# Kernel tuning notes

Measured on AMD Instinct MI355X. Metric: run time of the kernel, lower is better.

The kernel has to match this reference:

```python
import jax, jax.numpy as jnp
import numpy as np

D_MODEL = 2048
HQ = 32
HK = 8
DK = D_MODEL // HQ  # 64
G = HQ // HK        # 4
VOCAB = 32000
B, S = 1, 2048


def setup_inputs() -> dict:
    key = jax.random.key(0)
    ks = jax.random.split(key, 7)
    scale = 1.0 / np.sqrt(D_MODEL)
    X = jax.random.randint(ks[0], (B, S), 0, VOCAB, dtype=jnp.int64)
    emb = jax.random.normal(ks[1], (VOCAB, D_MODEL), dtype=jnp.float32)
    Wk = jax.random.normal(ks[2], (HK * DK, D_MODEL), dtype=jnp.float32) * scale
    Wv = jax.random.normal(ks[3], (HK * DK, D_MODEL), dtype=jnp.float32) * scale
    Wq = jax.random.normal(ks[4], (D_MODEL, D_MODEL), dtype=jnp.float32) * scale
    Wo_w = jax.random.normal(ks[5], (D_MODEL, D_MODEL), dtype=jnp.float32) * scale
    Wo_b = jax.random.normal(ks[6], (D_MODEL,), dtype=jnp.float32) * scale
    return {"X": X, "emb": emb, "Wk": Wk, "Wv": Wv, "Wq": Wq, "Wo_w": Wo_w, "Wo_b": Wo_b}


def reference(X, emb, Wk, Wv, Wq, Wo_w, Wo_b):
    e = emb[X]  # [B,S,D]
    b, s, _ = e.shape
    # torch Linear: y = x @ W.T (weights stored [out,in])
    k = (e @ Wk.T).reshape(b, s, HK, DK)            # [B,S,Hk,dk]
    v = (e @ Wv.T).reshape(b, s, HK, DK)            # [B,S,Hk,dk]
    q = (e @ Wq.T).reshape(b, s, HK, G, DK)         # q head index = i*G + g
    # scores: [B,Hk,G,S,S] — same math as expanding KV to Hq heads, no copy
    scores = jnp.einsum('bsigd,btid->bigst', q, k) / jnp.sqrt(jnp.asarray(DK, e.dtype))
    w = jax.nn.softmax(scores, axis=-1)
    ctx = jnp.einsum('bigst,btid->bsigd', w, v).reshape(b, s, D_MODEL)
    return ctx @ Wo_w.T + Wo_b
```

## Files before the change

kernel.cpp:

```cpp
#include <hip/hip_runtime.h>


typedef __bf16 bf16x8 __attribute__((ext_vector_type(8)));
typedef float f32x4 __attribute__((ext_vector_type(4)));
typedef float f32x16 __attribute__((ext_vector_type(16)));
typedef unsigned short ushort8_t __attribute__((ext_vector_type(8)));
typedef unsigned int uint4_t __attribute__((ext_vector_type(4)));

#define DEVI static __device__ __forceinline__

DEVI unsigned short f2bf(float f) {
    union { float f; unsigned int u; } c; c.f = f;
    unsigned int u = c.u;
    unsigned int r = (u + 0x7FFFu + ((u >> 16) & 1u)) >> 16;
    return (unsigned short)r;
}

DEVI f32x4 mfma16(bf16x8 a, bf16x8 b, f32x4 c) {
    return __builtin_amdgcn_mfma_f32_16x16x32_bf16(a, b, c, 0, 0, 0);
}
DEVI f32x16 mfma32(bf16x8 a, bf16x8 b, f32x16 c) {
    return __builtin_amdgcn_mfma_f32_32x32x16_bf16(a, b, c, 0, 0, 0);
}
DEVI unsigned cvtpk(float a, float b) {
    unsigned r;
    asm("v_cvt_pk_bf16_f32 %0, %1, %2" : "=v"(r) : "v"(a), "v"(b));
    return r;
}
DEVI void plswap(unsigned& a, unsigned& b) {
    asm("v_permlane32_swap_b32 %0, %1" : "+v"(a), "+v"(b));
}
DEVI void gload16(const unsigned short* g, unsigned short* l) {
    __builtin_amdgcn_global_load_lds(
        (const __attribute__((address_space(1))) void*)g,
        (__attribute__((address_space(3))) void*)l, 16, 0, 0);
}
#define WAIT_VM(n) asm volatile("s_waitcnt vmcnt(" #n ")" ::: "memory")
#define WAIT_LGKM0() asm volatile("s_waitcnt lgkmcnt(0)" ::: "memory")
#define BAR() __builtin_amdgcn_s_barrier()

DEVI void cvt8(const float* src, unsigned short* dst) {
    float4 f0 = *(const float4*)(src);
    float4 f1 = *(const float4*)(src + 4);
    ushort8_t v;
    v[0] = f2bf(f0.x); v[1] = f2bf(f0.y); v[2] = f2bf(f0.z); v[3] = f2bf(f0.w);
    v[4] = f2bf(f1.x); v[5] = f2bf(f1.y); v[6] = f2bf(f1.z); v[7] = f2bf(f1.w);
    *(ushort8_t*)(dst) = v;
}

__global__ __launch_bounds__(256)
void prep_k(const int* __restrict__ X, const float* __restrict__ emb,
            unsigned short* __restrict__ e,
            const float* __restrict__ Wk, unsigned short* __restrict__ Wkb,
            const float* __restrict__ Wv, unsigned short* __restrict__ Wvb,
            const float* __restrict__ Wq, unsigned short* __restrict__ Wqb,
            const float* __restrict__ Wo, unsigned short* __restrict__ Wob) {
    int b = blockIdx.x;
    if (b < 2048) {
        long long row = X[b];
        cvt8(emb + row * 2048 + threadIdx.x * 8, e + (size_t)b * 2048 + threadIdx.x * 8);
        return;
    }
    b -= 2048;
    const float* s; unsigned short* d; int off;
    if (b < 512) { s = Wk; d = Wkb; off = b; }
    else if (b < 1024) { s = Wv; d = Wvb; off = b - 512; }
    else if (b < 3072) { s = Wq; d = Wqb; off = b - 1024; }
    else { s = Wo; d = Wob; off = b - 3072; }
    size_t idx = ((size_t)off * 256 + threadIdx.x) * 8;
    cvt8(s + idx, d + idx);
}

template<int OM0, int OM1, int OM2>
__global__ __launch_bounds__(256)
void gemm_swz_k(const unsigned short* __restrict__ A,
                const unsigned short* __restrict__ W0, const unsigned short* __restrict__ W1,
                const unsigned short* __restrict__ W2,
                void* __restrict__ C0, void* __restrict__ C1, void* __restrict__ C2,
                int t1, int t2, int ldc0, int ldc1, int ldc2,
                const float* __restrict__ bias) {
    __shared__ unsigned short As[2 * 128 * 64];
    __shared__ unsigned short Bs[2 * 128 * 64];
    const int cpx = gridDim.x >> 3;
    int id = blockIdx.x;
    int swz = (id & 7) * cpx + (id >> 3);
    const int bx = swz & 15;
    const int by = swz >> 4;
    const unsigned short* Wp; void* Cp; int ldc, om, nb;
    if (by < t1)      { Wp = W0; Cp = C0; ldc = ldc0; om = OM0; nb = by; }
    else if (by < t2) { Wp = W1; Cp = C1; ldc = ldc1; om = OM1; nb = by - t1; }
    else              { Wp = W2; Cp = C2; ldc = ldc2; om = OM2; nb = by - t2; }
    const int m0 = bx * 128, n0 = nb * 128;
    const int tid = threadIdx.x, lane = tid & 63, w = tid >> 6;
    const int wm = (w >> 1) * 64, wn = (w & 1) * 64;
    const int lr = lane & 15, lg = lane >> 4;
    const int srow = tid >> 3, sj = tid & 7;

    f32x4 acc[4][4];
    #pragma unroll
    for (int i = 0; i < 4; i++)
        #pragma unroll
        for (int j = 0; j < 4; j++) acc[i][j] = {};

    #define G_STAGE(buf, k0)                                                          \
        _Pragma("unroll")                                                             \
        for (int i = 0; i < 4; i++) {                                                 \
            int row = srow + i * 32;                                                  \
            int jj = sj ^ (row & 7);                                                  \
            unsigned short* ad = As + (buf) * 8192 + (w * 64 + i * 256) * 8;          \
            unsigned short* bd = Bs + (buf) * 8192 + (w * 64 + i * 256) * 8;          \
            gload16(A  + (size_t)(m0 + row) * 2048 + (k0) + jj * 8, ad);              \
            gload16(Wp + (size_t)(n0 + row) * 2048 + (k0) + jj * 8, bd);              \
        }

    G_STAGE(0, 0);
    for (int s = 0; s < 32; ++s) {
        const int cur = s & 1;
        if (s < 31) {
            G_STAGE(cur ^ 1, (s + 1) * 64);
            WAIT_VM(8);
        } else {
            WAIT_VM(0);
        }
        BAR();
        const unsigned short* Asb = As + cur * 8192;
        const unsigned short* Bsb = Bs + cur * 8192;
        #pragma unroll
        for (int kk = 0; kk < 2; kk++) {
            bf16x8 af[4], bfr[4];
            #pragma unroll
            for (int mi = 0; mi < 4; mi++) {
                int r = wm + mi * 16 + lr;
                int g = (kk * 4 + lg) ^ (r & 7);
                af[mi] = *(const bf16x8*)(&Asb[r * 64 + g * 8]);
            }
            #pragma unroll
            for (int ni = 0; ni < 4; ni++) {
                int r = wn + ni * 16 + lr;
                int g = (kk * 4 + lg) ^ (r & 7);
                bfr[ni] = *(const bf16x8*)(&Bsb[r * 64 + g * 8]);
            }
            __builtin_amdgcn_s_setprio(1);
            #pragma unroll
            for (int mi = 0; mi < 4; mi++)
                #pragma unroll
                for (int ni = 0; ni < 4; ni++)
                    acc[mi][ni] = mfma16(af[mi], bfr[ni], acc[mi][ni]);
            __builtin_amdgcn_s_setprio(0);
        }
        WAIT_LGKM0();
        BAR();
    }
    #undef G_STAGE

    #pragma unroll
    for (int mi = 0; mi < 4; mi++)
        #pragma unroll
        for (int ni = 0; ni < 4; ni++) {
            int col = n0 + wn + ni * 16 + lr;
            #pragma unroll
            for (int jj = 0; jj < 4; jj++) {
                int rowg = m0 + wm + mi * 16 + lg * 4 + jj;
                float vv = acc[mi][ni][jj];
                if (om == 0) {
                    ((unsigned short*)Cp)[(size_t)rowg * ldc + col] = f2bf(vv);
                } else if (om == 1) {
                    ((float*)Cp)[(size_t)rowg * ldc + col] = vv + bias[col];
                } else {
                    ((unsigned short*)Cp)[(size_t)col * ldc + rowg] = f2bf(vv);
                }
            }
        }
}

__global__ __launch_bounds__(256)
void attn2_k(const unsigned short* __restrict__ Qb, const unsigned short* __restrict__ Kb,
             const unsigned short* __restrict__ VbT, unsigned short* __restrict__ Ctx) {
    __shared__ unsigned short Ks[2 * 64 * 64];
    __shared__ unsigned short Vts[2 * 64 * 64];
    int id = blockIdx.x;
    int swz = (id & 7) * 64 + (id >> 3);
    const int hq = swz >> 4;
    const int qt = swz & 15;
    const int ikv = hq >> 2;
    const int tid = threadIdx.x, lane = tid & 63, w = tid >> 6;
    const int l31 = lane & 31, hi = lane >> 5;
    const int qrow = qt * 128 + w * 32 + l31;
    const float CS = 0.125f * 1.44269504088896f;
    const int srow = tid >> 3, sj = tid & 7;

    bf16x8 qf[4];
    #pragma unroll
    for (int ks = 0; ks < 4; ks++)
        qf[ks] = *(const bf16x8*)(Qb + (size_t)qrow * 2048 + hq * 64 + ks * 16 + hi * 8);

    f32x16 oacc0 = {}, oacc1 = {};
    float m = -1e30f, l = 0.0f;

    #define A_STAGE(buf, t0)                                                          \
        _Pragma("unroll")                                                             \
        for (int i = 0; i < 2; i++) {                                                 \
            int row = srow + i * 32;                                                  \
            int jj = sj ^ (row & 7);                                                  \
            unsigned short* kd = Ks + (buf) * 4096 + (w * 64 + i * 256) * 8;          \
            unsigned short* vd = Vts + (buf) * 4096 + (w * 64 + i * 256) * 8;         \
            gload16(Kb + (size_t)((t0) + row) * 512 + ikv * 64 + jj * 8, kd);         \
            gload16(VbT + (size_t)(ikv * 64 + row) * 2048 + (t0) + jj * 8, vd);       \
        }

    A_STAGE(0, 0);
    for (int t = 0; t < 32; ++t) {
        const int cur = t & 1;
        if (t < 31) {
            A_STAGE(cur ^ 1, (t + 1) * 64);
            WAIT_VM(4);
        } else {
            WAIT_VM(0);
        }
        BAR();
        const unsigned short* Ksb = Ks + cur * 4096;
        const unsigned short* Vsb = Vts + cur * 4096;

        f32x16 s0 = {}, s1 = {};
        __builtin_amdgcn_s_setprio(1);
        #pragma unroll
        for (int ks = 0; ks < 4; ks++) {
            int gr = (2 * ks + hi) ^ (l31 & 7);
            bf16x8 kf0 = *(const bf16x8*)(&Ksb[l31 * 64 + gr * 8]);
            bf16x8 kf1 = *(const bf16x8*)(&Ksb[(32 + l31) * 64 + gr * 8]);
            s0 = mfma32(kf0, qf[ks], s0);
            s1 = mfma32(kf1, qf[ks], s1);
        }
        __builtin_amdgcn_s_setprio(0);

        float mx[8];
        #pragma unroll
        for (int r = 0; r < 8; r++)
            mx[r] = fmaxf(fmaxf(s0[2 * r], s0[2 * r + 1]),
                          fmaxf(s1[2 * r], s1[2 * r + 1]));
        #pragma unroll
        for (int st = 4; st > 0; st >>= 1)
            #pragma unroll
            for (int r = 0; r < st; r++) mx[r] = fmaxf(mx[r], mx[r + st]);
        float pmax = fmaxf(mx[0], __shfl_xor(mx[0], 32, 64));
        pmax *= CS;

        if (!__all(pmax <= m + 8.0f)) {
            float mnew = fmaxf(m, pmax);
            float sc = exp2f(m - mnew);
            m = mnew;
            l *= sc;
            #pragma unroll
            for (int r = 0; r < 16; r++) {
                const int qp = (r & 3) + 8 * (r >> 2);
                float scv = __shfl(sc, qp + 4 * hi, 64);
                oacc0[r] *= scv;
                oacc1[r] *= scv;
            }
        }

        float rs0 = 0.f, rs1 = 0.f, rs2 = 0.f, rs3 = 0.f;
        #pragma unroll
        for (int r = 0; r < 16; r += 4) {
            float p0 = exp2f(__builtin_fmaf(s0[r],     CS, -m)); s0[r]     = p0; rs0 += p0;
            float p1 = exp2f(__builtin_fmaf(s0[r + 1], CS, -m)); s0[r + 1] = p1; rs1 += p1;
            float p2 = exp2f(__builtin_fmaf(s0[r + 2], CS, -m)); s0[r + 2] = p2; rs2 += p2;
            float p3 = exp2f(__builtin_fmaf(s0[r + 3], CS, -m)); s0[r + 3] = p3; rs3 += p3;
        }
        #pragma unroll
        for (int r = 0; r < 16; r += 4) {
            float p0 = exp2f(__builtin_fmaf(s1[r],     CS, -m)); s1[r]     = p0; rs0 += p0;
            float p1 = exp2f(__builtin_fmaf(s1[r + 1], CS, -m)); s1[r + 1] = p1; rs1 += p1;
            float p2 = exp2f(__builtin_fmaf(s1[r + 2], CS, -m)); s1[r + 2] = p2; rs2 += p2;
            float p3 = exp2f(__builtin_fmaf(s1[r + 3], CS, -m)); s1[r + 3] = p3; rs3 += p3;
        }
        float rs = (rs0 + rs1) + (rs2 + rs3);
        rs += __shfl_xor(rs, 32, 64);
        l += rs;

        uint4_t pw[4];
        #pragma unroll
        for (int c = 0; c < 2; c++) {
            unsigned a   = cvtpk(s0[8 * c + 0], s0[8 * c + 1]);
            unsigned bb  = cvtpk(s0[8 * c + 2], s0[8 * c + 3]);
            unsigned cc2 = cvtpk(s0[8 * c + 4], s0[8 * c + 5]);
            unsigned dd  = cvtpk(s0[8 * c + 6], s0[8 * c + 7]);
            plswap(a, cc2); plswap(bb, dd);
            pw[c][0] = a; pw[c][1] = bb; pw[c][2] = cc2; pw[c][3] = dd;
        }
        #pragma unroll
        for (int c = 0; c < 2; c++) {
            unsigned a   = cvtpk(s1[8 * c + 0], s1[8 * c + 1]);
            unsigned bb  = cvtpk(s1[8 * c + 2], s1[8 * c + 3]);
            unsigned cc2 = cvtpk(s1[8 * c + 4], s1[8 * c + 5]);
            unsigned dd  = cvtpk(s1[8 * c + 6], s1[8 * c + 7]);
            plswap(a, cc2); plswap(bb, dd);
            pw[2 + c][0] = a; pw[2 + c][1] = bb; pw[2 + c][2] = cc2; pw[2 + c][3] = dd;
        }

        __builtin_amdgcn_s_setprio(1);
        #pragma unroll
        for (int ks = 0; ks < 4; ks++) {
            bf16x8 pa = __builtin_bit_cast(bf16x8, pw[ks]);
            int gr = (2 * ks + hi) ^ (l31 & 7);
            bf16x8 vf0 = *(const bf16x8*)(&Vsb[l31 * 64 + gr * 8]);
            bf16x8 vf1 = *(const bf16x8*)(&Vsb[(32 + l31) * 64 + gr * 8]);
            oacc0 = mfma32(pa, vf0, oacc0);
            oacc1 = mfma32(pa, vf1, oacc1);
        }
        __builtin_amdgcn_s_setprio(0);
        WAIT_LGKM0();
        BAR();
    }
    #undef A_STAGE

    float linv = 1.0f / l;
    #pragma unroll
    for (int r = 0; r < 16; r++) {
        const int qp = (r & 3) + 8 * (r >> 2);
        float lv = __shfl(linv, qp + 4 * hi, 64);
        int row = qt * 128 + w * 32 + qp + 4 * hi;
        Ctx[(size_t)row * 2048 + hq * 64 + l31]      = f2bf(oacc0[r] * lv);
        Ctx[(size_t)row * 2048 + hq * 64 + 32 + l31] = f2bf(oacc1[r] * lv);
    }
}

extern "C" void kernel_launch(void* const* d_in, const int* in_sizes, int n_in,
                              void* d_out, int out_size, void* d_ws, size_t ws_size,
                              hipStream_t stream) {
    (void)in_sizes; (void)n_in; (void)out_size; (void)ws_size;
    const int*   X   = (const int*)d_in[0];
    const float* emb = (const float*)d_in[1];
    const float* Wk  = (const float*)d_in[2];
    const float* Wv  = (const float*)d_in[3];
    const float* Wq  = (const float*)d_in[4];
    const float* Wo  = (const float*)d_in[5];
    const float* Wb  = (const float*)d_in[6];

    unsigned short* e   = (unsigned short*)d_ws;
    unsigned short* Kb  = e   + (size_t)2048 * 2048;
    unsigned short* VbT = Kb  + (size_t)2048 * 512;
    unsigned short* Qb  = VbT + (size_t)512 * 2048;
    unsigned short* Ctx = Qb  + (size_t)2048 * 2048;
    unsigned short* Wkb = Ctx + (size_t)2048 * 2048;
    unsigned short* Wvb = Wkb + (size_t)512 * 2048;
    unsigned short* Wqb = Wvb + (size_t)512 * 2048;
    unsigned short* Wob = Wqb + (size_t)2048 * 2048;

    prep_k<<<dim3(2048 + 5120), dim3(256), 0, stream>>>(X, emb, e, Wk, Wkb, Wv, Wvb,
                                                        Wq, Wqb, Wo, Wob);
    gemm_swz_k<0, 0, 2><<<dim3(384), dim3(256), 0, stream>>>(
        e, Wqb, Wkb, Wvb, (void*)Qb, (void*)Kb, (void*)VbT,
        16, 20, 2048, 512, 2048, nullptr);
    attn2_k<<<dim3(512), dim3(256), 0, stream>>>(Qb, Kb, VbT, Ctx);
    gemm_swz_k<1, 1, 1><<<dim3(256), dim3(256), 0, stream>>>(
        Ctx, Wob, Wob, Wob, d_out, d_out, d_out,
        16, 32, 2048, 2048, 2048, Wb);
}
```

Before: 166.2 us.

## Fold softmax scale into Q projection and compute row sums via MFMA

```diff
diff --git a/kernel.cpp b/kernel.cpp
--- a/kernel.cpp
+++ b/kernel.cpp
@@ -8,6 +8,8 @@
 typedef unsigned int uint4_t __attribute__((ext_vector_type(4)));
 
 #define DEVI static __device__ __forceinline__
+
+#define QSCALE 0.180336880111112f
 
 DEVI unsigned short f2bf(float f) {
     union { float f; unsigned int u; } c; c.f = f;
@@ -166,8 +168,10 @@
                     ((unsigned short*)Cp)[(size_t)rowg * ldc + col] = f2bf(vv);
                 } else if (om == 1) {
                     ((float*)Cp)[(size_t)rowg * ldc + col] = vv + bias[col];
+                } else if (om == 2) {
+                    ((unsigned short*)Cp)[(size_t)col * ldc + rowg] = f2bf(vv);
                 } else {
-                    ((unsigned short*)Cp)[(size_t)col * ldc + rowg] = f2bf(vv);
+                    ((unsigned short*)Cp)[(size_t)rowg * ldc + col] = f2bf(vv * QSCALE);
                 }
             }
         }
@@ -186,7 +190,6 @@
     const int tid = threadIdx.x, lane = tid & 63, w = tid >> 6;
     const int l31 = lane & 31, hi = lane >> 5;
     const int qrow = qt * 128 + w * 32 + l31;
-    const float CS = 0.125f * 1.44269504088896f;
     const int srow = tid >> 3, sj = tid & 7;
 
     bf16x8 qf[4];
@@ -194,8 +197,12 @@
     for (int ks = 0; ks < 4; ks++)
         qf[ks] = *(const bf16x8*)(Qb + (size_t)qrow * 2048 + hq * 64 + ks * 16 + hi * 8);
 
-    f32x16 oacc0 = {}, oacc1 = {};
-    float m = -1e30f, l = 0.0f;
+    bf16x8 onesb;
+    #pragma unroll
+    for (int i = 0; i < 8; i++) onesb[i] = (__bf16)1.0f;
+
+    f32x16 oacc0 = {}, oacc1 = {}, lacc = {};
+    float m = -1e30f;
 
     #define A_STAGE(buf, t0)                                                          \
         _Pragma("unroll")                                                             \
@@ -233,50 +240,43 @@
         }
         __builtin_amdgcn_s_setprio(0);
 
-        float mx[8];
-        #pragma unroll
-        for (int r = 0; r < 8; r++)
-            mx[r] = fmaxf(fmaxf(s0[2 * r], s0[2 * r + 1]),
-                          fmaxf(s1[2 * r], s1[2 * r + 1]));
-        #pragma unroll
-        for (int st = 4; st > 0; st >>= 1)
-            #pragma unroll
-            for (int r = 0; r < st; r++) mx[r] = fmaxf(mx[r], mx[r + st]);
-        float pmax = fmaxf(mx[0], __shfl_xor(mx[0], 32, 64));
-        pmax *= CS;
+        float a0 = fmaxf(fmaxf(s0[0],  s0[1]),  s0[2]);
+        float a1 = fmaxf(fmaxf(s0[3],  s0[4]),  s0[5]);
+        float a2 = fmaxf(fmaxf(s0[6],  s0[7]),  s0[8]);
+        float a3 = fmaxf(fmaxf(s0[9],  s0[10]), s0[11]);
+        float a4 = fmaxf(fmaxf(s0[12], s0[13]), s0[14]);
+        float b0 = fmaxf(fmaxf(s1[0],  s1[1]),  s1[2]);
+        float b1 = fmaxf(fmaxf(s1[3],  s1[4]),  s1[5]);
+        float b2 = fmaxf(fmaxf(s1[6],  s1[7]),  s1[8]);
+        float b3 = fmaxf(fmaxf(s1[9],  s1[10]), s1[11]);
+        float b4 = fmaxf(fmaxf(s1[12], s1[13]), s1[14]);
+        float c0 = fmaxf(s0[15], s1[15]);
+        float d0 = fmaxf(fmaxf(a0, a1), a2);
+        float d1 = fmaxf(fmaxf(a3, a4), b0);
+        float d2 = fmaxf(fmaxf(b1, b2), b3);
+        float d3 = fmaxf(fmaxf(b4, c0), d0);
+        float pmax = fmaxf(fmaxf(d1, d2), d3);
+        pmax = fmaxf(pmax, __shfl_xor(pmax, 32, 64));
 
         if (!__all(pmax <= m + 8.0f)) {
             float mnew = fmaxf(m, pmax);
             float sc = exp2f(m - mnew);
             m = mnew;
-            l *= sc;
             #pragma unroll
             for (int r = 0; r < 16; r++) {
                 const int qp = (r & 3) + 8 * (r >> 2);
                 float scv = __shfl(sc, qp + 4 * hi, 64);
                 oacc0[r] *= scv;
                 oacc1[r] *= scv;
+                lacc[r] *= scv;
             }
         }
 
-        float rs0 = 0.f, rs1 = 0.f, rs2 = 0.f, rs3 = 0.f;
-        #pragma unroll
-        for (int r = 0; r < 16; r += 4) {
-            float p0 = exp2f(__builtin_fmaf(s0[r],     CS, -m)); s0[r]     = p0; rs0 += p0;
-            float p1 = exp2f(__builtin_fmaf(s0[r + 1], CS, -m)); s0[r + 1] = p1; rs1 += p1;
-            float p2 = exp2f(__builtin_fmaf(s0[r + 2], CS, -m)); s0[r + 2] = p2; rs2 += p2;
-            float p3 = exp2f(__builtin_fmaf(s0[r + 3], CS, -m)); s0[r + 3] = p3; rs3 += p3;
-        }
-        #pragma unroll
-        for (int r = 0; r < 16; r += 4) {
-            float p0 = exp2f(__builtin_fmaf(s1[r],     CS, -m)); s1[r]     = p0; rs0 += p0;
-            float p1 = exp2f(__builtin_fmaf(s1[r + 1], CS, -m)); s1[r + 1] = p1; rs1 += p1;
-            float p2 = exp2f(__builtin_fmaf(s1[r + 2], CS, -m)); s1[r + 2] = p2; rs2 += p2;
-            float p3 = exp2f(__builtin_fmaf(s1[r + 3], CS, -m)); s1[r + 3] = p3; rs3 += p3;
-        }
-        float rs = (rs0 + rs1) + (rs2 + rs3);
-        rs += __shfl_xor(rs, 32, 64);
-        l += rs;
+        #pragma unroll
+        for (int r = 0; r < 16; r++) {
+            s0[r] = exp2f(s0[r] - m);
+            s1[r] = exp2f(s1[r] - m);
+        }
 
         uint4_t pw[4];
         #pragma unroll
@@ -307,6 +307,7 @@
             bf16x8 vf1 = *(const bf16x8*)(&Vsb[(32 + l31) * 64 + gr * 8]);
             oacc0 = mfma32(pa, vf0, oacc0);
             oacc1 = mfma32(pa, vf1, oacc1);
+            lacc  = mfma32(pa, onesb, lacc);
         }
         __builtin_amdgcn_s_setprio(0);
         WAIT_LGKM0();
@@ -314,12 +315,10 @@
     }
     #undef A_STAGE
 
-    float linv = 1.0f / l;
     #pragma unroll
     for (int r = 0; r < 16; r++) {
-        const int qp = (r & 3) + 8 * (r >> 2);
-        float lv = __shfl(linv, qp + 4 * hi, 64);
-        int row = qt * 128 + w * 32 + qp + 4 * hi;
+        float lv = 1.0f / lacc[r];
+        int row = qt * 128 + w * 32 + (r & 3) + 8 * (r >> 2) + 4 * hi;
         Ctx[(size_t)row * 2048 + hq * 64 + l31]      = f2bf(oacc0[r] * lv);
         Ctx[(size_t)row * 2048 + hq * 64 + 32 + l31] = f2bf(oacc1[r] * lv);
     }
@@ -349,7 +348,7 @@
 
     prep_k<<<dim3(2048 + 5120), dim3(256), 0, stream>>>(X, emb, e, Wk, Wkb, Wv, Wvb,
                                                         Wq, Wqb, Wo, Wob);
-    gemm_swz_k<0, 0, 2><<<dim3(384), dim3(256), 0, stream>>>(
+    gemm_swz_k<3, 0, 2><<<dim3(384), dim3(256), 0, stream>>>(
         e, Wqb, Wkb, Wvb, (void*)Qb, (void*)Kb, (void*)VbT,
         16, 20, 2048, 512, 2048, nullptr);
     attn2_k<<<dim3(512), dim3(256), 0, stream>>>(Qb, Kb, VbT, Ctx);
```

Result: faster. 162.9 us (-2.0%).
